# Optimization experiments

Measured on AMD Instinct MI355X. Metric: run time of the kernel, lower is better.

Reference implementation:

```python
import jax, jax.numpy as jnp
import numpy as np

B, T = 16, 2048
N_PROBLEMS, N_KCS, N_HIDDEN = 10000, 64, 128


def setup_inputs() -> dict:
    key = jax.random.key(0)
    ks = jax.random.split(key, 9)
    y = (jax.random.uniform(ks[0], (B, T)) > 0.5).astype(jnp.float32)  # binary responses
    problem_seq = jax.random.randint(ks[1], (B, T), 0, N_PROBLEMS)
    # soft assignment matrix (rows roughly on the simplex, like gumbel_softmax output)
    A = jax.nn.softmax(jax.random.normal(ks[2], (N_PROBLEMS, N_KCS)), axis=1)
    kc_embd_w = jax.random.normal(ks[3], (N_KCS, N_HIDDEN)) * 0.1
    lam_w = jax.random.normal(ks[4], (N_HIDDEN, 1)) * 0.02
    lam_b = jnp.zeros((1,), jnp.float32)
    guess_w = jax.random.normal(ks[5], (N_HIDDEN, 1)) * 0.1
    guess_b = jnp.zeros((1,), jnp.float32)
    slip_w = jax.random.normal(ks[6], (N_HIDDEN, 1)) * 0.1
    slip_b = jnp.zeros((1,), jnp.float32)
    return {"y": y, "problem_seq": problem_seq, "A": A,
            "kc_embd_w": kc_embd_w, "lam_w": lam_w, "lam_b": lam_b,
            "guess_w": guess_w, "guess_b": guess_b,
            "slip_w": slip_w, "slip_b": slip_b}


def reference(y, problem_seq, A, kc_embd_w, lam_w, lam_b, guess_w, guess_b, slip_w, slip_b):
    x = A[problem_seq]                                   # [B,T,K]
    sim = jnp.einsum('btk,bsk->bts', x, x)               # [B,T,T]
    t = sim.shape[1]
    mask = jnp.tril(jnp.ones((t, t), sim.dtype), k=-1)   # strictly past
    sim = sim * mask
    # reversed cumsum along last axis: cumsum from the right
    delta_t = jnp.flip(jnp.cumsum(jnp.flip(sim, axis=2), axis=2), axis=2)
    kc = x @ kc_embd_w                                   # [B,T,H]
    kc_lam = jnp.exp(kc @ lam_w + lam_b)                 # [B,T,1]
    weight = sim * jnp.exp(-kc_lam * delta_t)            # [B,T,T]
    weight_normed = weight / (jnp.sum(weight, axis=2, keepdims=True) + 1e-6)
    h = jnp.sum(y[:, None, :] * weight_normed, axis=2)   # [B,T]
    guess = jax.nn.sigmoid(kc @ guess_w + guess_b)[:, :, 0]
    slip = jax.nn.sigmoid(kc @ slip_w + slip_b)[:, :, 0]
    yhat = h * (1 - slip) + (1 - h) * guess
    return jnp.clip(yhat, 0.01, 0.99)
```

## Files before the change

### kernel.cpp

```cpp
#include <hip/hip_runtime.h>

#define B_ 16
#define T_ 2048
#define NP 10000
#define NH 128

#define XF_F   0
#define NLAM_F 2097152
#define GG_F   2129920
#define SS_F   2162688

typedef __attribute__((ext_vector_type(8))) short bf16x8;
typedef __attribute__((ext_vector_type(4))) float f32x4;

__device__ __forceinline__ unsigned short f2bf(float x) {
  unsigned u = __float_as_uint(x);
  u += 0x7FFFu + ((u >> 16) & 1u);
  return (unsigned short)(u >> 16);
}
__device__ __forceinline__ size_t xfbase(int b, int R, int plane, int ks) {
  return ((((size_t)b * 128 + R) * 2 + plane) * 2 + ks) * 512;
}

__global__ __launch_bounds__(256) void prep(
    const int* __restrict__ pseq, const float* __restrict__ A,
    const float* __restrict__ kcw,
    const float* __restrict__ lam_w, const float* __restrict__ lam_b,
    const float* __restrict__ guess_w, const float* __restrict__ guess_b,
    const float* __restrict__ slip_w, const float* __restrict__ slip_b,
    float* __restrict__ ws) {
  const int tid = threadIdx.x, bid = blockIdx.x;
  const int lane = tid & 63, wv = tid >> 6;
  {
    const int W = bid * 4 + wv;
    const int b = W >> 8, rem = W & 255, R = rem >> 1, ks = rem & 1;
    const int row = (R << 4) + (lane & 15), gp = lane >> 4;
    const float* src = A + (size_t)pseq[b * T_ + row] * 64 + ks * 32 + gp * 8;
    float4 v0 = *(const float4*)src;
    float4 v1 = *(const float4*)(src + 4);
    float vv[8] = {v0.x, v0.y, v0.z, v0.w, v1.x, v1.y, v1.z, v1.w};
    union { unsigned short s[8]; bf16x8 v; } H, L;
    #pragma unroll
    for (int i = 0; i < 8; ++i) {
      H.s[i] = f2bf(vv[i]);
      float e = vv[i] - __uint_as_float((unsigned)H.s[i] << 16);
      L.s[i] = f2bf(e);
    }
    unsigned short* X = (unsigned short*)ws;
    *(bf16x8*)(X + xfbase(b, R, 0, ks) + lane * 8) = H.v;
    *(bf16x8*)(X + xfbase(b, R, 1, ks) + lane * 8) = L.v;
  }
  if (bid < 128) {
    __shared__ float wvec[3][64];
    if (tid < 192) {
      int vec = tid >> 6, k = tid & 63;
      const float* wvp = (vec == 0) ? lam_w : (vec == 1 ? guess_w : slip_w);
      float acc = 0.f;
      #pragma unroll 8
      for (int h = 0; h < NH; ++h) acc = fmaf(kcw[k * NH + h], wvp[h], acc);
      wvec[vec][k] = acc;
    }
    __syncthreads();
    const int tg = bid * 256 + tid;
    const float* xr = A + ((size_t)pseq[tg] << 6);
    float aL = 0.f, aG = 0.f, aS = 0.f;
    #pragma unroll
    for (int k = 0; k < 64; ++k) {
      float xv = xr[k];
      aL = fmaf(xv, wvec[0][k], aL);
      aG = fmaf(xv, wvec[1][k], aG);
      aS = fmaf(xv, wvec[2][k], aS);
    }
    ws[NLAM_F + tg] = -__expf(aL + lam_b[0]);
    ws[GG_F + tg]   = 1.f / (1.f + __expf(-(aG + guess_b[0])));
    ws[SS_F + tg]   = 1.f / (1.f + __expf(-(aS + slip_b[0])));
  }
}

__global__ __launch_bounds__(512, 2) void mainK(
    const float* __restrict__ y, float* __restrict__ ws,
    float* __restrict__ out) {
  __shared__ float part[8][3][64];
  const int tid = threadIdx.x, bid = blockIdx.x;
  const int lane = tid & 63;
  const int wv = __builtin_amdgcn_readfirstlane(tid >> 6);
  const int u = bid & 255, half = bid >> 8;
  const int b = u >> 4, kk = u & 15;
  const int tile = half ? kk : 31 - kk;
  const int t0 = tile << 6, base = b * T_;
  const int c = lane & 15, g = lane >> 4;
  const unsigned short* X = (const unsigned short*)ws;

  float nl[4];
  #pragma unroll
  for (int fj = 0; fj < 4; ++fj) nl[fj] = ws[NLAM_F + base + t0 + 16 * fj + c];

  const int nchunks = tile + 1;
  const int nc = (nchunks + 7) >> 3;
  const int cLo = wv * nc;
  const int cHi = min(cLo + nc, nchunks);

  float NA[4] = {0,0,0,0}, DA[4] = {0,0,0,0}, RA[4] = {0,0,0,0};

  for (int cc = cHi - 1; cc >= cLo; --cc) {
    const bool diag = (cc == tile);
    float yy[4][4];
    #pragma unroll
    for (int fi = 0; fi < 4; ++fi) {
      float4 t4 = *(const float4*)(y + base + (cc << 6) + 16 * fi + 4 * g);
      yy[fi][0] = t4.x; yy[fi][1] = t4.y; yy[fi][2] = t4.z; yy[fi][3] = t4.w;
    }
    #pragma unroll
    for (int fjh = 0; fjh < 2; ++fjh) {
      bf16x8 bh[2][2], bm[2][2];
      #pragma unroll
      for (int j2 = 0; j2 < 2; ++j2)
        #pragma unroll
        for (int ks = 0; ks < 2; ++ks) {
          const int R = tile * 4 + 2 * fjh + j2;
          bh[j2][ks] = *(const bf16x8*)(X + xfbase(b, R, 0, ks) + lane * 8);
          bm[j2][ks] = *(const bf16x8*)(X + xfbase(b, R, 1, ks) + lane * 8);
        }
      f32x4 acc[4][2] = {};
      #pragma unroll
      for (int ks = 0; ks < 2; ++ks) {
        bf16x8 ah[4], am[4];
        #pragma unroll
        for (int fi = 0; fi < 4; ++fi) {
          const int R = cc * 4 + fi;
          ah[fi] = *(const bf16x8*)(X + xfbase(b, R, 0, ks) + lane * 8);
          am[fi] = *(const bf16x8*)(X + xfbase(b, R, 1, ks) + lane * 8);
        }
        #pragma unroll
        for (int fi = 0; fi < 4; ++fi)
          #pragma unroll
          for (int j2 = 0; j2 < 2; ++j2) {
            acc[fi][j2] = __builtin_amdgcn_mfma_f32_16x16x32_bf16(ah[fi], bh[j2][ks], acc[fi][j2], 0, 0, 0);
            acc[fi][j2] = __builtin_amdgcn_mfma_f32_16x16x32_bf16(ah[fi], bm[j2][ks], acc[fi][j2], 0, 0, 0);
            acc[fi][j2] = __builtin_amdgcn_mfma_f32_16x16x32_bf16(am[fi], bh[j2][ks], acc[fi][j2], 0, 0, 0);
          }
      }
      #pragma unroll
      for (int j2 = 0; j2 < 2; ++j2) {
        const int fj = 2 * fjh + j2;
        float sm[4][4], pp[4][4], S[4], ft[4];
        #pragma unroll
        for (int fi = 0; fi < 4; ++fi) {
          f32x4 v = acc[fi][j2];
          if (diag) {
            #pragma unroll
            for (int rr = 0; rr < 4; ++rr)
              if (16 * fi + 4 * g + rr >= 16 * fj + c) v[rr] = 0.f;
          }
          sm[fi][0]=v.x; sm[fi][1]=v.y; sm[fi][2]=v.z; sm[fi][3]=v.w;
          float p3 = v.w, p2 = p3 + v.z, p1 = p2 + v.y, p0 = p1 + v.x;
          pp[fi][0]=p0; pp[fi][1]=p1; pp[fi][2]=p2; pp[fi][3]=p3;
          float u16 = __shfl_xor(p0, 16);
          float pr = p0 + u16;
          float u32 = __shfl_xor(pr, 32);
          ft[fi] = pr + u32;
          S[fi] = ((g & 1) ? 0.f : u16) + ((g < 2) ? u32 : 0.f);
        }
        const float F2 = ft[3], F1 = F2 + ft[2], F0 = F1 + ft[1];
        const float Fv[4] = {F0, F1, F2, 0.f};
        float num = 0.f, den = 0.f;
        #pragma unroll
        for (int fi = 0; fi < 4; ++fi) {
          const float SF = S[fi] + Fv[fi];
          #pragma unroll
          for (int rr = 0; rr < 4; ++rr) {
            const float dl = pp[fi][rr] + SF;
            const float e = __expf(nl[fj] * dl);
            const float w = sm[fi][rr] * e;
            den += w;
            num = fmaf(yy[fi][rr], w, num);
          }
        }
        num += __shfl_xor(num, 16); num += __shfl_xor(num, 32);
        den += __shfl_xor(den, 16); den += __shfl_xor(den, 32);
        const float tot = Fv[0] + ft[0];
        const float e = __expf(nl[fj] * RA[fj]);
        NA[fj] = fmaf(num, e, NA[fj]);
        DA[fj] = fmaf(den, e, DA[fj]);
        RA[fj] += tot;
      }
    }
  }

  if (g == 0) {
    #pragma unroll
    for (int fj = 0; fj < 4; ++fj) {
      part[wv][0][16 * fj + c] = NA[fj];
      part[wv][1][16 * fj + c] = DA[fj];
      part[wv][2][16 * fj + c] = RA[fj];
    }
  }
  __syncthreads();

  if (wv == 0) {
    const int t = t0 + lane;
    const float nlt = ws[NLAM_F + base + t];
    float N = 0.f, D = 0.f, Roff = 0.f;
    #pragma unroll
    for (int w = 7; w >= 0; --w) {
      const float e = __expf(nlt * Roff);
      N = fmaf(part[w][0][lane], e, N);
      D = fmaf(part[w][1][lane], e, D);
      Roff += part[w][2][lane];
    }
    const float gv = ws[GG_F + base + t];
    const float sv = ws[SS_F + base + t];
    const float h = N / (D + 1e-6f);
    float yh = h * (1.f - sv) + (1.f - h) * gv;
    out[base + t] = fminf(fmaxf(yh, 0.01f), 0.99f);
  }
}

extern "C" void kernel_launch(void* const* d_in, const int* in_sizes, int n_in,
                              void* d_out, int out_size, void* d_ws, size_t ws_size,
                              hipStream_t stream) {
  const float* y    = (const float*)d_in[0];
  const int*   pseq = (const int*)  d_in[1];
  const float* A    = (const float*)d_in[2];
  const float* kcw  = (const float*)d_in[3];
  const float* lw   = (const float*)d_in[4];
  const float* lb   = (const float*)d_in[5];
  const float* gw   = (const float*)d_in[6];
  const float* gb   = (const float*)d_in[7];
  const float* sw   = (const float*)d_in[8];
  const float* sb   = (const float*)d_in[9];
  float* out = (float*)d_out;
  float* ws  = (float*)d_ws;

  prep<<<1024, 256, 0, stream>>>(pseq, A, kcw, lw, lb, gw, gb, sw, sb, ws);
  mainK<<<512, 512, 0, stream>>>(y, ws, out);
}
```

Baseline: 121.1 us.

## Use single fp16 MFMA instead of split bf16 hi/lo products for similarity

Replaces the three-MFMA bf16 hi/lo split (hi*hi + hi*lo + lo*hi) with one fp16 MFMA per tile, and stores a single fp16 plane of gathered A rows. This cuts matrix-core work by about a factor of three and halves the operand traffic, at the cost of lower accuracy in the similarity values. It also stages y through LDS per wave, recomputes the masked prefix sums instead of keeping them in arrays, and raises launch bounds to 4 blocks per CU so register pressure drops and occupancy rises.

```diff
diff --git a/kernel.cpp b/kernel.cpp
--- a/kernel.cpp
+++ b/kernel.cpp
@@ -6,20 +6,15 @@
 #define NH 128
 
 #define XF_F   0
-#define NLAM_F 2097152
-#define GG_F   2129920
-#define SS_F   2162688
-
-typedef __attribute__((ext_vector_type(8))) short bf16x8;
+#define NLAM_F 1048576
+#define GG_F   1081344
+#define SS_F   1114112
+
+typedef __attribute__((ext_vector_type(8))) _Float16 f16x8;
 typedef __attribute__((ext_vector_type(4))) float f32x4;
 
-__device__ __forceinline__ unsigned short f2bf(float x) {
-  unsigned u = __float_as_uint(x);
-  u += 0x7FFFu + ((u >> 16) & 1u);
-  return (unsigned short)(u >> 16);
-}
-__device__ __forceinline__ size_t xfbase(int b, int R, int plane, int ks) {
-  return ((((size_t)b * 128 + R) * 2 + plane) * 2 + ks) * 512;
+__device__ __forceinline__ size_t xfbase(int b, int R, int ks) {
+  return (((size_t)b * 128 + R) * 2 + ks) * 512;
 }
 
 __global__ __launch_bounds__(256) void prep(
@@ -39,16 +34,10 @@
     float4 v0 = *(const float4*)src;
     float4 v1 = *(const float4*)(src + 4);
     float vv[8] = {v0.x, v0.y, v0.z, v0.w, v1.x, v1.y, v1.z, v1.w};
-    union { unsigned short s[8]; bf16x8 v; } H, L;
-    #pragma unroll
-    for (int i = 0; i < 8; ++i) {
-      H.s[i] = f2bf(vv[i]);
-      float e = vv[i] - __uint_as_float((unsigned)H.s[i] << 16);
-      L.s[i] = f2bf(e);
-    }
-    unsigned short* X = (unsigned short*)ws;
-    *(bf16x8*)(X + xfbase(b, R, 0, ks) + lane * 8) = H.v;
-    *(bf16x8*)(X + xfbase(b, R, 1, ks) + lane * 8) = L.v;
+    union { _Float16 h[8]; f16x8 v; } H;
+    #pragma unroll
+    for (int i = 0; i < 8; ++i) H.h[i] = (_Float16)vv[i];
+    *(f16x8*)((unsigned short*)ws + xfbase(b, R, ks) + lane * 8) = H.v;
   }
   if (bid < 128) {
     __shared__ float wvec[3][64];
@@ -77,10 +66,11 @@
   }
 }
 
-__global__ __launch_bounds__(512, 2) void mainK(
+__global__ __launch_bounds__(512, 4) void mainK(
     const float* __restrict__ y, float* __restrict__ ws,
     float* __restrict__ out) {
   __shared__ float part[8][3][64];
+  __shared__ float yl[8][64];
   const int tid = threadIdx.x, bid = blockIdx.x;
   const int lane = tid & 63;
   const int wv = __builtin_amdgcn_readfirstlane(tid >> 6);
@@ -104,46 +94,30 @@
 
   for (int cc = cHi - 1; cc >= cLo; --cc) {
     const bool diag = (cc == tile);
-    float yy[4][4];
-    #pragma unroll
-    for (int fi = 0; fi < 4; ++fi) {
-      float4 t4 = *(const float4*)(y + base + (cc << 6) + 16 * fi + 4 * g);
-      yy[fi][0] = t4.x; yy[fi][1] = t4.y; yy[fi][2] = t4.z; yy[fi][3] = t4.w;
-    }
+    yl[wv][lane] = y[base + (cc << 6) + lane];
+
     #pragma unroll
     for (int fjh = 0; fjh < 2; ++fjh) {
-      bf16x8 bh[2][2], bm[2][2];
-      #pragma unroll
-      for (int j2 = 0; j2 < 2; ++j2)
-        #pragma unroll
-        for (int ks = 0; ks < 2; ++ks) {
-          const int R = tile * 4 + 2 * fjh + j2;
-          bh[j2][ks] = *(const bf16x8*)(X + xfbase(b, R, 0, ks) + lane * 8);
-          bm[j2][ks] = *(const bf16x8*)(X + xfbase(b, R, 1, ks) + lane * 8);
-        }
       f32x4 acc[4][2] = {};
       #pragma unroll
       for (int ks = 0; ks < 2; ++ks) {
-        bf16x8 ah[4], am[4];
-        #pragma unroll
-        for (int fi = 0; fi < 4; ++fi) {
-          const int R = cc * 4 + fi;
-          ah[fi] = *(const bf16x8*)(X + xfbase(b, R, 0, ks) + lane * 8);
-          am[fi] = *(const bf16x8*)(X + xfbase(b, R, 1, ks) + lane * 8);
-        }
+        f16x8 bfr[2], afr[4];
+        #pragma unroll
+        for (int j2 = 0; j2 < 2; ++j2)
+          bfr[j2] = *(const f16x8*)(X + xfbase(b, tile * 4 + 2 * fjh + j2, ks) + lane * 8);
+        #pragma unroll
+        for (int fi = 0; fi < 4; ++fi)
+          afr[fi] = *(const f16x8*)(X + xfbase(b, cc * 4 + fi, ks) + lane * 8);
         #pragma unroll
         for (int fi = 0; fi < 4; ++fi)
           #pragma unroll
-          for (int j2 = 0; j2 < 2; ++j2) {
-            acc[fi][j2] = __builtin_amdgcn_mfma_f32_16x16x32_bf16(ah[fi], bh[j2][ks], acc[fi][j2], 0, 0, 0);
-            acc[fi][j2] = __builtin_amdgcn_mfma_f32_16x16x32_bf16(ah[fi], bm[j2][ks], acc[fi][j2], 0, 0, 0);
-            acc[fi][j2] = __builtin_amdgcn_mfma_f32_16x16x32_bf16(am[fi], bh[j2][ks], acc[fi][j2], 0, 0, 0);
-          }
+          for (int j2 = 0; j2 < 2; ++j2)
+            acc[fi][j2] = __builtin_amdgcn_mfma_f32_16x16x32_f16(afr[fi], bfr[j2], acc[fi][j2], 0, 0, 0);
       }
       #pragma unroll
       for (int j2 = 0; j2 < 2; ++j2) {
         const int fj = 2 * fjh + j2;
-        float sm[4][4], pp[4][4], S[4], ft[4];
+        float S[4], ft[4];
         #pragma unroll
         for (int fi = 0; fi < 4; ++fi) {
           f32x4 v = acc[fi][j2];
@@ -152,12 +126,10 @@
             for (int rr = 0; rr < 4; ++rr)
               if (16 * fi + 4 * g + rr >= 16 * fj + c) v[rr] = 0.f;
           }
-          sm[fi][0]=v.x; sm[fi][1]=v.y; sm[fi][2]=v.z; sm[fi][3]=v.w;
-          float p3 = v.w, p2 = p3 + v.z, p1 = p2 + v.y, p0 = p1 + v.x;
-          pp[fi][0]=p0; pp[fi][1]=p1; pp[fi][2]=p2; pp[fi][3]=p3;
-          float u16 = __shfl_xor(p0, 16);
-          float pr = p0 + u16;
-          float u32 = __shfl_xor(pr, 32);
+          const float p0 = ((v.x + v.y) + (v.z + v.w));
+          const float u16 = __shfl_xor(p0, 16);
+          const float pr = p0 + u16;
+          const float u32 = __shfl_xor(pr, 32);
           ft[fi] = pr + u32;
           S[fi] = ((g & 1) ? 0.f : u16) + ((g < 2) ? u32 : 0.f);
         }
@@ -166,14 +138,22 @@
         float num = 0.f, den = 0.f;
         #pragma unroll
         for (int fi = 0; fi < 4; ++fi) {
+          f32x4 v = acc[fi][j2];
+          if (diag) {
+            #pragma unroll
+            for (int rr = 0; rr < 4; ++rr)
+              if (16 * fi + 4 * g + rr >= 16 * fj + c) v[rr] = 0.f;
+          }
           const float SF = S[fi] + Fv[fi];
+          float p3 = v.w, p2 = p3 + v.z, p1 = p2 + v.y, p0 = p1 + v.x;
+          const float pp[4] = {p0, p1, p2, p3};
+          const float sm[4] = {v.x, v.y, v.z, v.w};
           #pragma unroll
           for (int rr = 0; rr < 4; ++rr) {
-            const float dl = pp[fi][rr] + SF;
-            const float e = __expf(nl[fj] * dl);
-            const float w = sm[fi][rr] * e;
+            const float e = __expf(nl[fj] * (pp[rr] + SF));
+            const float w = sm[rr] * e;
             den += w;
-            num = fmaf(yy[fi][rr], w, num);
+            num = fmaf(yl[wv][16 * fi + 4 * g + rr], w, num);
           }
         }
         num += __shfl_xor(num, 16); num += __shfl_xor(num, 32);
```

New measurement: 160.7 us. 32.6% more time.
